# Kernel optimization log

Measured on AMD Instinct MI355X. Metric: run time of the kernel, lower is better.

## Reference

```python
import jax, jax.numpy as jnp
import numpy as np

HEADS = 16
DIM_HEAD = 64
SCALE = DIM_HEAD ** -0.5
EPS = 1e-5


def _vdp_linear(mu, sigma, Wmu, Wsig_raw):
    # y = W x with W ~ N(Wmu, softplus(Wsig_raw)), x ~ N(mu, sigma) (diag covs):
    # Var(y) = (mu^2 + sigma) @ Wsig^T + sigma @ (Wmu^2)^T
    Wsig = jax.nn.softplus(Wsig_raw)
    mu_y = mu @ Wmu.T
    sigma_y = (mu * mu + sigma) @ Wsig.T + sigma @ (Wmu * Wmu).T
    return mu_y, sigma_y


def _vdp_layernorm(mu, sigma, gamma, beta):
    mean = jnp.mean(mu, axis=-1, keepdims=True)
    var = jnp.var(mu, axis=-1, keepdims=True)
    inv = 1.0 / jnp.sqrt(var + EPS)
    mu_y = (mu - mean) * inv * gamma + beta
    # first-order variance propagation through the affine normalization
    sigma_y = sigma * (gamma * gamma) * (inv * inv)
    return mu_y, sigma_y


def _vdp_softmax(mu, sigma):
    p = jax.nn.softmax(mu, axis=-1)
    # diagonal-Jacobian approximation: J_ii = p_i(1-p_i)
    J = p * (1.0 - p)
    return p, (J * J) * sigma


def setup_inputs() -> dict:
    key = jax.random.key(0)
    ks = jax.random.split(key, 6)
    B, N, D = 4, 1024, 1024
    inner = HEADS * DIM_HEAD  # 1024
    w_std = 0.02
    return {
        "mu": jax.random.normal(ks[0], (B, N, D), jnp.float32),
        "sigma": jax.random.uniform(ks[1], (B, N, D), jnp.float32),
        "ln_gamma": jnp.ones((D,), jnp.float32),
        "ln_beta": jnp.zeros((D,), jnp.float32),
        "Wqkv_mu": w_std * jax.random.normal(ks[2], (3 * inner, D), jnp.float32),
        "Wqkv_sigma_raw": -5.0 + 0.1 * jax.random.normal(ks[3], (3 * inner, D), jnp.float32),
        "Wout_mu": w_std * jax.random.normal(ks[4], (D, inner), jnp.float32),
        "Wout_sigma_raw": -5.0 + 0.1 * jax.random.normal(ks[5], (D, inner), jnp.float32),
    }


def reference(mu, sigma, ln_gamma, ln_beta, Wqkv_mu, Wqkv_sigma_raw, Wout_mu, Wout_sigma_raw):
    B, N, D = mu.shape

    mu_n, sigma_n = _vdp_layernorm(mu, sigma, ln_gamma, ln_beta)
    mu_qkv, sigma_qkv = _vdp_linear(mu_n, sigma_n, Wqkv_mu, Wqkv_sigma_raw)

    def split_heads(t):
        q, k, v = jnp.split(t, 3, axis=-1)
        rs = lambda a: a.reshape(B, N, HEADS, DIM_HEAD).transpose(0, 2, 1, 3)
        return rs(q), rs(k), rs(v)

    mu_q, mu_k, mu_v = split_heads(mu_qkv)
    sg_q, sg_k, sg_v = split_heads(sigma_qkv)

    mu_dots = jnp.einsum("bhid,bhjd->bhij", mu_q, mu_k) * SCALE
    sg_dots = jnp.einsum("bhid,bhjd->bhij", sg_q, sg_k) * SCALE

    mu_attn, sg_attn = _vdp_softmax(mu_dots, sg_dots)

    mu_o = jnp.einsum("bhij,bhjd->bhid", mu_attn, mu_v)
    sg_o = jnp.einsum("bhij,bhjd->bhid", sg_attn, sg_v)

    merge = lambda t: t.transpose(0, 2, 1, 3).reshape(B, N, HEADS * DIM_HEAD)
    mu_o, sg_o = merge(mu_o), merge(sg_o)

    return _vdp_linear(mu_o, sg_o, Wout_mu, Wout_sigma_raw)
```

## Files before the change

kernel.cpp:

```cpp
#include <hip/hip_runtime.h>

typedef unsigned short u16;
typedef unsigned int u32;
typedef __bf16 bf16x8 __attribute__((ext_vector_type(8)));
typedef float f32x4 __attribute__((ext_vector_type(4)));

__device__ __forceinline__ float b2f(u16 u) { return __uint_as_float(((u32)u) << 16); }
__device__ __forceinline__ u16 f2b(float f) {
  u32 u = __float_as_uint(f);
  u += 0x7fffu + ((u >> 16) & 1u);
  return (u16)(u >> 16);
}

__device__ __forceinline__ void gll16(const u16* g, u16* l) {
  __builtin_amdgcn_global_load_lds(
      (const __attribute__((address_space(1))) void*)g,
      (__attribute__((address_space(3))) void*)l, 16, 0, 0);
}

__device__ __forceinline__ float4 load4(const void* p, size_t idx, bool f32) {
  if (f32) return *(const float4*)((const float*)p + idx);
  ushort4 u = *(const ushort4*)((const u16*)p + idx);
  return make_float4(b2f(u.x), b2f(u.y), b2f(u.z), b2f(u.w));
}

__global__ __launch_bounds__(256) void detect_kernel(const u16* __restrict__ sig,
                                                     int* __restrict__ flag) {
  __shared__ int cnt;
  if (threadIdx.x == 0) cnt = 0;
  __syncthreads();
  int c = 0;
  for (int i = threadIdx.x; i < 65536; i += 256) {
    u16 v = sig[i];
    c += ((v & 0x7F80u) == 0x7F80u) ? 1 : 0;
  }
  atomicAdd(&cnt, c);
  __syncthreads();
  if (threadIdx.x == 0) *flag = (cnt >= 8) ? 1 : 0;
}

__device__ __forceinline__ float block_sum(float v, float* red, int t) {
  red[t] = v; __syncthreads();
  #pragma unroll
  for (int s = 128; s > 0; s >>= 1) {
    if (t < s) red[t] += red[t + s];
    __syncthreads();
  }
  float r = red[0];
  __syncthreads();
  return r;
}

__global__ __launch_bounds__(256) void ln_prep_kernel(
    const int* __restrict__ flag,
    const void* __restrict__ mu, const void* __restrict__ sigma,
    const void* __restrict__ gamma, const void* __restrict__ beta,
    u16* __restrict__ mu_n, u16* __restrict__ a1sg)
{
  __shared__ float red[256];
  const bool f32 = (*flag != 0);
  const int t = threadIdx.x;
  const size_t base = (size_t)blockIdx.x * 1024 + (size_t)t * 4;
  float4 xm = load4(mu, base, f32);
  float4 xs = load4(sigma, base, f32);
  float x0 = xm.x, x1 = xm.y, x2 = xm.z, x3 = xm.w;
  float s0 = xs.x, s1 = xs.y, s2 = xs.z, s3 = xs.w;

  float sum = block_sum(x0 + x1 + x2 + x3, red, t);
  float ssq = block_sum(x0*x0 + x1*x1 + x2*x2 + x3*x3, red, t);
  float mean = sum * (1.0f / 1024.0f);
  float var  = ssq * (1.0f / 1024.0f) - mean * mean;
  float inv  = 1.0f / sqrtf(var + 1e-5f);
  float inv2 = inv * inv;

  float4 g4 = load4(gamma, (size_t)t * 4, f32);
  float4 b4 = load4(beta, (size_t)t * 4, f32);

  float m0 = (x0 - mean) * inv * g4.x + b4.x;
  float m1 = (x1 - mean) * inv * g4.y + b4.y;
  float m2 = (x2 - mean) * inv * g4.z + b4.z;
  float m3 = (x3 - mean) * inv * g4.w + b4.w;
  float v0 = s0 * g4.x * g4.x * inv2;
  float v1 = s1 * g4.y * g4.y * inv2;
  float v2 = s2 * g4.z * g4.z * inv2;
  float v3 = s3 * g4.w * g4.w * inv2;

  ushort4 omu = { f2b(m0), f2b(m1), f2b(m2), f2b(m3) };
  ushort4 oa1 = { f2b(m0*m0 + v0), f2b(m1*m1 + v1), f2b(m2*m2 + v2), f2b(m3*m3 + v3) };
  ushort4 osg = { f2b(v0), f2b(v1), f2b(v2), f2b(v3) };
  *(ushort4*)(mu_n + base) = omu;
  size_t r2 = (size_t)blockIdx.x * 2048 + (size_t)t * 4;
  *(ushort4*)(a1sg + r2) = oa1;
  *(ushort4*)(a1sg + r2 + 1024) = osg;
}

__global__ __launch_bounds__(256) void wprep_kernel(
    const int* __restrict__ flag,
    const void* __restrict__ wmu, const void* __restrict__ wsraw,
    u16* __restrict__ obf, u16* __restrict__ os2, int n)
{
  const bool f32 = (*flag != 0);
  size_t idx = ((size_t)blockIdx.x * 256 + threadIdx.x) * 4;
  if (idx >= (size_t)n) return;
  int row = (int)(idx >> 10), k = (int)(idx & 1023);
  float4 m4 = load4(wmu, idx, f32);
  float4 s4 = load4(wsraw, idx, f32);
  float m[4] = { m4.x, m4.y, m4.z, m4.w };
  float s[4] = { s4.x, s4.y, s4.z, s4.w };
  ushort4 ob, os, oq;
  u16* obp = (u16*)&ob; u16* osp = (u16*)&os; u16* oqp = (u16*)&oq;
  #pragma unroll
  for (int i = 0; i < 4; ++i) {
    float sp = (s[i] > 15.f) ? s[i] : log1pf(__expf(s[i]));
    obp[i] = f2b(m[i]);
    osp[i] = f2b(sp);
    oqp[i] = f2b(m[i] * m[i]);
  }
  *(ushort4*)(obf + idx) = ob;
  size_t r2 = (size_t)row * 2048 + k;
  *(ushort4*)(os2 + r2) = os;
  *(ushort4*)(os2 + r2 + 1024) = oq;
}

template<bool DYN>
__global__ __launch_bounds__(256) void gemm_pair_kernel(
    const u16* __restrict__ A0, const u16* __restrict__ B0, int K0, void* C0, size_t ob0,
    const u16* __restrict__ A1, const u16* __restrict__ B1, int K1, void* C1, size_t ob1,
    int split, int N, const int* __restrict__ flag)
{
  __shared__ u16 lA[128 * 64];
  __shared__ u16 lB[128 * 64];
  const int t = threadIdx.x;
  int bx = blockIdx.x;
  const u16 *A, *B; void* C; size_t obase; int K;
  if (bx < split) { A = A0; B = B0; K = K0; C = C0; obase = ob0; }
  else { bx -= split; A = A1; B = B1; K = K1; C = C1; obase = ob1; }

  const int n0 = bx * 128, m0 = blockIdx.y * 128;
  const int lane = t & 63, wave = t >> 6;
  const int wr = (wave >> 1) * 64, wc = (wave & 1) * 64;
  const int ml = lane & 15, qd = lane >> 4;

  const int srow = t >> 3;
  const int gseg = (t & 7) ^ (srow & 7);
  const int mlx = ml & 7;

  f32x4 acc[4][4];
  #pragma unroll
  for (int i = 0; i < 4; ++i)
    #pragma unroll
    for (int j = 0; j < 4; ++j) acc[i][j] = (f32x4){0.f, 0.f, 0.f, 0.f};

  for (int k0 = 0; k0 < K; k0 += 64) {
    __syncthreads();
    #pragma unroll
    for (int rep = 0; rep < 4; ++rep) {
      gll16(A + (size_t)(m0 + srow + rep * 32) * K + k0 + gseg * 8,
            lA + rep * 2048 + wave * 512);
      gll16(B + (size_t)(n0 + srow + rep * 32) * K + k0 + gseg * 8,
            lB + rep * 2048 + wave * 512);
    }
    __syncthreads();
    #pragma unroll
    for (int kk = 0; kk < 2; ++kk) {
      bf16x8 af[4], bfr[4];
      #pragma unroll
      for (int ti = 0; ti < 4; ++ti)
        af[ti] = *(const bf16x8*)&lA[(wr + ti * 16 + ml) * 64 + (((kk * 4 + qd) ^ mlx)) * 8];
      #pragma unroll
      for (int tj = 0; tj < 4; ++tj)
        bfr[tj] = *(const bf16x8*)&lB[(wc + tj * 16 + ml) * 64 + (((kk * 4 + qd) ^ mlx)) * 8];
      #pragma unroll
      for (int ti = 0; ti < 4; ++ti)
        #pragma unroll
        for (int tj = 0; tj < 4; ++tj)
          acc[ti][tj] = __builtin_amdgcn_mfma_f32_16x16x32_bf16(af[ti], bfr[tj], acc[ti][tj], 0, 0, 0);
    }
  }

  const bool of32 = DYN && (*flag != 0);
  #pragma unroll
  for (int ti = 0; ti < 4; ++ti) {
    int row = m0 + wr + ti * 16 + qd * 4;
    #pragma unroll
    for (int tj = 0; tj < 4; ++tj) {
      int col = n0 + wc + tj * 16 + ml;
      #pragma unroll
      for (int r = 0; r < 4; ++r) {
        float v = acc[ti][tj][r];
        size_t off = obase + (size_t)(row + r) * N + col;
        if (DYN) {
          if (of32) ((float*)C)[off] = v;
          else      ((u16*)C)[off] = f2b(v);
        } else {
          ((u16*)C)[off] = f2b(v);
        }
      }
    }
  }
}

__global__ __launch_bounds__(512, 4) void attn_kernel(
    const u16* __restrict__ qkv_mu, const u16* __restrict__ qkv_sg,
    u16* __restrict__ o_mu, u16* __restrict__ a1sgo)
{
  __shared__ u16 lKW[128 * 72];
  __shared__ u16 lV[128 * 72];
  __shared__ u16 lP[128 * 72];

  const int t = threadIdx.x;
  const int wv = t >> 6, lane = t & 63;
  const int ml = lane & 15, qd = lane >> 4;
  const int b = blockIdx.y >> 4, h = blockIdx.y & 15;
  const size_t rowbase = (size_t)b * 1024 * 3072;
  const int i0 = blockIdx.x * 128;
  const int qcol = h * 64, kcol = 1024 + h * 64, vcol = 2048 + h * 64;
  const int qrow = wv * 16;

  bf16x8 aQm[2], aQs[2];
  #pragma unroll
  for (int ks = 0; ks < 2; ++ks) {
    size_t ga = rowbase + (size_t)(i0 + qrow + ml) * 3072 + qcol + ks * 32 + qd * 8;
    aQm[ks] = *(const bf16x8*)(qkv_mu + ga);
    aQs[ks] = *(const bf16x8*)(qkv_sg + ga);
  }

  float mfin[4], lacc[4];
  #pragma unroll
  for (int r = 0; r < 4; ++r) { mfin[r] = -1e30f; lacc[r] = 0.f; }

  for (int j0 = 0; j0 < 1024; j0 += 128) {
    __syncthreads();
    #pragma unroll
    for (int rep = 0; rep < 2; ++rep) {
      int c = t + rep * 512;
      int row = c >> 3, seg = c & 7;
      *(uint4*)&lKW[row * 72 + seg * 8] =
          *(const uint4*)(qkv_mu + rowbase + (size_t)(j0 + row) * 3072 + kcol + seg * 8);
    }
    __syncthreads();
    f32x4 s8[8];
    #pragma unroll
    for (int tj = 0; tj < 8; ++tj) {
      bf16x8 b0 = *(const bf16x8*)&lKW[(tj * 16 + ml) * 72 + qd * 8];
      bf16x8 b1 = *(const bf16x8*)&lKW[(tj * 16 + ml) * 72 + 32 + qd * 8];
      f32x4 s = (f32x4){0.f, 0.f, 0.f, 0.f};
      s = __builtin_amdgcn_mfma_f32_16x16x32_bf16(aQm[0], b0, s, 0, 0, 0);
      s = __builtin_amdgcn_mfma_f32_16x16x32_bf16(aQm[1], b1, s, 0, 0, 0);
      s8[tj] = s;
    }
    #pragma unroll
    for (int r = 0; r < 4; ++r) {
      float nm = mfin[r];
      #pragma unroll
      for (int tj = 0; tj < 8; ++tj) nm = fmaxf(nm, s8[tj][r] * 0.125f);
      float add = 0.f;
      #pragma unroll
      for (int tj = 0; tj < 8; ++tj) add += __expf(s8[tj][r] * 0.125f - nm);
      lacc[r] = lacc[r] * __expf(mfin[r] - nm) + add;
      mfin[r] = nm;
    }
  }
  #pragma unroll
  for (int r = 0; r < 4; ++r) {
    float m = mfin[r], l = lacc[r];
    #pragma unroll
    for (int xo = 1; xo < 16; xo <<= 1) {
      float om = __shfl_xor(m, xo, 64);
      float ol = __shfl_xor(l, xo, 64);
      float nm = fmaxf(m, om);
      l = l * __expf(m - nm) + ol * __expf(om - nm);
      m = nm;
    }
    mfin[r] = m;
    lacc[r] = 1.0f / l;
  }

  f32x4 accm[4], accs[4];
  #pragma unroll
  for (int tj = 0; tj < 4; ++tj) {
    accm[tj] = (f32x4){0.f, 0.f, 0.f, 0.f};
    accs[tj] = (f32x4){0.f, 0.f, 0.f, 0.f};
  }

  for (int j0 = 0; j0 < 1024; j0 += 64) {
    __syncthreads();
    #pragma unroll
    for (int rep = 0; rep < 2; ++rep) {
      int c = t + rep * 512;
      int row = c >> 3, seg = c & 7;
      const u16* src = (row < 64) ? qkv_mu : qkv_sg;
      int rr = row & 63;
      *(uint4*)&lKW[row * 72 + seg * 8] =
          *(const uint4*)(src + rowbase + (size_t)(j0 + rr) * 3072 + kcol + seg * 8);
    }
    {
      int buf = t >> 8, rem = t & 255;
      int db = rem >> 4, tb = rem & 15;
      const u16* src = buf ? qkv_sg : qkv_mu;
      ushort4 vals[4];
      #pragma unroll
      for (int i = 0; i < 4; ++i)
        vals[i] = *(const ushort4*)(src + rowbase + (size_t)(j0 + tb * 4 + i) * 3072 + vcol + db * 4);
      #pragma unroll
      for (int k = 0; k < 4; ++k) {
        ushort4 o;
        u16* op = (u16*)&o;
        const u16* v0 = (const u16*)&vals[0];
        const u16* v1 = (const u16*)&vals[1];
        const u16* v2 = (const u16*)&vals[2];
        const u16* v3 = (const u16*)&vals[3];
        op[0] = v0[k]; op[1] = v1[k]; op[2] = v2[k]; op[3] = v3[k];
        *(ushort4*)&lV[(buf * 64 + db * 4 + k) * 72 + tb * 4] = o;
      }
    }
    __syncthreads();

    f32x4 sm[4], ss[4];
    #pragma unroll
    for (int tj = 0; tj < 4; ++tj) {
      bf16x8 bm0 = *(const bf16x8*)&lKW[(tj * 16 + ml) * 72 + qd * 8];
      bf16x8 bm1 = *(const bf16x8*)&lKW[(tj * 16 + ml) * 72 + 32 + qd * 8];
      bf16x8 bs0 = *(const bf16x8*)&lKW[(64 + tj * 16 + ml) * 72 + qd * 8];
      bf16x8 bs1 = *(const bf16x8*)&lKW[(64 + tj * 16 + ml) * 72 + 32 + qd * 8];
      f32x4 s = (f32x4){0.f, 0.f, 0.f, 0.f};
      s = __builtin_amdgcn_mfma_f32_16x16x32_bf16(aQm[0], bm0, s, 0, 0, 0);
      s = __builtin_amdgcn_mfma_f32_16x16x32_bf16(aQm[1], bm1, s, 0, 0, 0);
      sm[tj] = s;
      f32x4 s2 = (f32x4){0.f, 0.f, 0.f, 0.f};
      s2 = __builtin_amdgcn_mfma_f32_16x16x32_bf16(aQs[0], bs0, s2, 0, 0, 0);
      s2 = __builtin_amdgcn_mfma_f32_16x16x32_bf16(aQs[1], bs1, s2, 0, 0, 0);
      ss[tj] = s2;
    }
    __syncthreads();

    #pragma unroll
    for (int tj = 0; tj < 4; ++tj)
      #pragma unroll
      for (int r = 0; r < 4; ++r) {
        float p = __expf(sm[tj][r] * 0.125f - mfin[r]) * lacc[r];
        float jp = p * (1.0f - p);
        float w = jp * jp * (ss[tj][r] * 0.125f);
        int row = qrow + qd * 4 + r;
        lP[row * 72 + tj * 16 + ml]  = f2b(p);
        lKW[row * 72 + tj * 16 + ml] = f2b(w);
      }
    __syncthreads();

    bf16x8 ap[2], aw[2];
    #pragma unroll
    for (int ks = 0; ks < 2; ++ks) {
      ap[ks] = *(const bf16x8*)&lP[(qrow + ml) * 72 + ks * 32 + qd * 8];
      aw[ks] = *(const bf16x8*)&lKW[(qrow + ml) * 72 + ks * 32 + qd * 8];
    }
    #pragma unroll
    for (int tj = 0; tj < 4; ++tj) {
      bf16x8 vm0 = *(const bf16x8*)&lV[(tj * 16 + ml) * 72 + qd * 8];
      bf16x8 vm1 = *(const bf16x8*)&lV[(tj * 16 + ml) * 72 + 32 + qd * 8];
      bf16x8 vs0 = *(const bf16x8*)&lV[(64 + tj * 16 + ml) * 72 + qd * 8];
      bf16x8 vs1 = *(const bf16x8*)&lV[(64 + tj * 16 + ml) * 72 + 32 + qd * 8];
      accm[tj] = __builtin_amdgcn_mfma_f32_16x16x32_bf16(ap[0], vm0, accm[tj], 0, 0, 0);
      accm[tj] = __builtin_amdgcn_mfma_f32_16x16x32_bf16(ap[1], vm1, accm[tj], 0, 0, 0);
      accs[tj] = __builtin_amdgcn_mfma_f32_16x16x32_bf16(aw[0], vs0, accs[tj], 0, 0, 0);
      accs[tj] = __builtin_amdgcn_mfma_f32_16x16x32_bf16(aw[1], vs1, accs[tj], 0, 0, 0);
    }
  }

  #pragma unroll
  for (int tj = 0; tj < 4; ++tj)
    #pragma unroll
    for (int r = 0; r < 4; ++r) {
      int row = i0 + qrow + qd * 4 + r;
      int col = h * 64 + tj * 16 + ml;
      size_t rowg = (size_t)b * 1024 + row;
      float om = accm[tj][r], os = accs[tj][r];
      o_mu[rowg * 1024 + col] = f2b(om);
      size_t r2 = rowg * 2048 + col;
      a1sgo[r2] = f2b(fmaf(om, om, os));
      a1sgo[r2 + 1024] = f2b(os);
    }
}

extern "C" void kernel_launch(void* const* d_in, const int* in_sizes, int n_in,
                              void* d_out, int out_size, void* d_ws, size_t ws_size,
                              hipStream_t stream)
{
  (void)in_sizes; (void)n_in; (void)out_size; (void)ws_size;
  const void* mu        = d_in[0];
  const void* sigma     = d_in[1];
  const void* gamma     = d_in[2];
  const void* beta      = d_in[3];
  const void* wqkv_mu   = d_in[4];
  const void* wqkv_sraw = d_in[5];
  const void* wout_mu   = d_in[6];
  const void* wout_sraw = d_in[7];

  u16* ws = (u16*)d_ws;
  const size_t R = 4096;
  u16* mu_n   = ws;
  u16* a1sg   = mu_n + R * 1024;
  u16* wq_bf  = a1sg + R * 2048;
  u16* wqs2   = wq_bf + 3072 * 1024;
  u16* wo_bf  = wqs2 + 3072 * 2048;
  u16* wos2   = wo_bf + 1024 * 1024;
  u16* mu_qkv = wos2 + 1024 * 2048;
  u16* sg_qkv = mu_qkv + R * 3072;
  int* flag   = (int*)(sg_qkv + R * 3072);

  u16* mu_o  = mu_n;
  u16* a1sgo = a1sg;

  detect_kernel<<<1, 256, 0, stream>>>((const u16*)sigma, flag);
  ln_prep_kernel<<<4096, 256, 0, stream>>>(flag, mu, sigma, gamma, beta, mu_n, a1sg);
  wprep_kernel<<<(3072 * 1024) / 1024, 256, 0, stream>>>(flag, wqkv_mu, wqkv_sraw,
                                                         wq_bf, wqs2, 3072 * 1024);
  wprep_kernel<<<(1024 * 1024) / 1024, 256, 0, stream>>>(flag, wout_mu, wout_sraw,
                                                         wo_bf, wos2, 1024 * 1024);

  gemm_pair_kernel<false><<<dim3(48, 32), 256, 0, stream>>>(
      mu_n, wq_bf, 1024, mu_qkv, 0,
      a1sg, wqs2, 2048, sg_qkv, 0,
      24, 3072, nullptr);

  attn_kernel<<<dim3(8, 64), 512, 0, stream>>>(mu_qkv, sg_qkv, mu_o, a1sgo);

  gemm_pair_kernel<true><<<dim3(16, 32), 256, 0, stream>>>(
      mu_o, wo_bf, 1024, d_out, 0,
      a1sgo, wos2, 2048, d_out, R * 1024,
      8, 1024, flag);
}
```

Before: 442.8 us.

## Split attention softmax normalizer into separate kernel without max subtraction

```diff
diff --git a/kernel.cpp b/kernel.cpp
--- a/kernel.cpp
+++ b/kernel.cpp
@@ -30,25 +30,13 @@
   if (threadIdx.x == 0) cnt = 0;
   __syncthreads();
   int c = 0;
-  for (int i = threadIdx.x; i < 65536; i += 256) {
+  for (int i = threadIdx.x; i < 16384; i += 256) {
     u16 v = sig[i];
     c += ((v & 0x7F80u) == 0x7F80u) ? 1 : 0;
   }
   atomicAdd(&cnt, c);
   __syncthreads();
   if (threadIdx.x == 0) *flag = (cnt >= 8) ? 1 : 0;
-}
-
-__device__ __forceinline__ float block_sum(float v, float* red, int t) {
-  red[t] = v; __syncthreads();
-  #pragma unroll
-  for (int s = 128; s > 0; s >>= 1) {
-    if (t < s) red[t] += red[t + s];
-    __syncthreads();
-  }
-  float r = red[0];
-  __syncthreads();
-  return r;
 }
 
 __global__ __launch_bounds__(256) void ln_prep_kernel(
@@ -57,17 +45,28 @@
     const void* __restrict__ gamma, const void* __restrict__ beta,
     u16* __restrict__ mu_n, u16* __restrict__ a1sg)
 {
-  __shared__ float red[256];
+  __shared__ float ps[4], pq[4];
   const bool f32 = (*flag != 0);
   const int t = threadIdx.x;
+  const int wv = t >> 6, lane = t & 63;
   const size_t base = (size_t)blockIdx.x * 1024 + (size_t)t * 4;
   float4 xm = load4(mu, base, f32);
   float4 xs = load4(sigma, base, f32);
   float x0 = xm.x, x1 = xm.y, x2 = xm.z, x3 = xm.w;
   float s0 = xs.x, s1 = xs.y, s2 = xs.z, s3 = xs.w;
 
-  float sum = block_sum(x0 + x1 + x2 + x3, red, t);
-  float ssq = block_sum(x0*x0 + x1*x1 + x2*x2 + x3*x3, red, t);
+  float sv = x0 + x1 + x2 + x3;
+  float qv = x0*x0 + x1*x1 + x2*x2 + x3*x3;
+  #pragma unroll
+  for (int off = 32; off > 0; off >>= 1) {
+    sv += __shfl_xor(sv, off, 64);
+    qv += __shfl_xor(qv, off, 64);
+  }
+  if (lane == 0) { ps[wv] = sv; pq[wv] = qv; }
+  __syncthreads();
+  float sum = ps[0] + ps[1] + ps[2] + ps[3];
+  float ssq = pq[0] + pq[1] + pq[2] + pq[3];
+
   float mean = sum * (1.0f / 1024.0f);
   float var  = ssq * (1.0f / 1024.0f) - mean * mean;
   float inv  = 1.0f / sqrtf(var + 1e-5f);
@@ -200,8 +199,62 @@
   }
 }
 
-__global__ __launch_bounds__(512, 4) void attn_kernel(
+__global__ __launch_bounds__(256) void attn_pass1(
+    const u16* __restrict__ qkv_mu, float* __restrict__ invl)
+{
+  __shared__ u16 lK[128 * 72];
+  const int t = threadIdx.x;
+  const int wv = t >> 6, lane = t & 63;
+  const int ml = lane & 15, qd = lane >> 4;
+  const int bh = blockIdx.y;
+  const int b = bh >> 4, h = bh & 15;
+  const size_t rowbase = (size_t)b * 1024 * 3072;
+  const int i0 = blockIdx.x * 64;
+  const int qcol = h * 64, kcol = 1024 + h * 64;
+  const int qrow = wv * 16;
+
+  bf16x8 aQm[2];
+  #pragma unroll
+  for (int ks = 0; ks < 2; ++ks)
+    aQm[ks] = *(const bf16x8*)(qkv_mu + rowbase +
+        (size_t)(i0 + qrow + ml) * 3072 + qcol + ks * 32 + qd * 8);
+
+  float lsum[4] = {0.f, 0.f, 0.f, 0.f};
+
+  for (int j0 = 0; j0 < 1024; j0 += 128) {
+    __syncthreads();
+    #pragma unroll
+    for (int rep = 0; rep < 4; ++rep) {
+      int c = t + rep * 256;
+      int row = c >> 3, seg = c & 7;
+      *(uint4*)&lK[row * 72 + seg * 8] =
+          *(const uint4*)(qkv_mu + rowbase + (size_t)(j0 + row) * 3072 + kcol + seg * 8);
+    }
+    __syncthreads();
+    #pragma unroll
+    for (int tj = 0; tj < 8; ++tj) {
+      bf16x8 b0 = *(const bf16x8*)&lK[(tj * 16 + ml) * 72 + qd * 8];
+      bf16x8 b1 = *(const bf16x8*)&lK[(tj * 16 + ml) * 72 + 32 + qd * 8];
+      f32x4 s = (f32x4){0.f, 0.f, 0.f, 0.f};
+      s = __builtin_amdgcn_mfma_f32_16x16x32_bf16(aQm[0], b0, s, 0, 0, 0);
+      s = __builtin_amdgcn_mfma_f32_16x16x32_bf16(aQm[1], b1, s, 0, 0, 0);
+      #pragma unroll
+      for (int r = 0; r < 4; ++r) lsum[r] += __expf(s[r] * 0.125f);
+    }
+  }
+  #pragma unroll
+  for (int r = 0; r < 4; ++r) {
+    float l = lsum[r];
+    #pragma unroll
+    for (int xo = 1; xo < 16; xo <<= 1) l += __shfl_xor(l, xo, 64);
+    if (ml == 0)
+      invl[(size_t)bh * 1024 + i0 + qrow + qd * 4 + r] = 1.0f / l;
+  }
+}
+
+__global__ __launch_bounds__(512, 4) void attn_pass2(
     const u16* __restrict__ qkv_mu, const u16* __restrict__ qkv_sg,
+    const float* __restrict__ invl,
     u16* __restrict__ o_mu, u16* __restrict__ a1sgo)
 {
   __shared__ u16 lKW[128 * 72];
@@ -211,7 +264,8 @@
   const int t = threadIdx.x;
   const int wv = t >> 6, lane = t & 63;
   const int ml = lane & 15, qd = lane >> 4;
-  const int b = blockIdx.y >> 4, h = blockIdx.y & 15;
+  const int bh = blockIdx.y;
+  const int b = bh >> 4, h = bh & 15;
   const size_t rowbase = (size_t)b * 1024 * 3072;
   const int i0 = blockIdx.x * 128;
   const int qcol = h * 64, kcol = 1024 + h * 64, vcol = 2048 + h * 64;
@@ -225,56 +279,10 @@
     aQs[ks] = *(const bf16x8*)(qkv_sg + ga);
   }
 
-  float mfin[4], lacc[4];
-  #pragma unroll
-  for (int r = 0; r < 4; ++r) { mfin[r] = -1e30f; lacc[r] = 0.f; }
-
-  for (int j0 = 0; j0 < 1024; j0 += 128) {
-    __syncthreads();
-    #pragma unroll
-    for (int rep = 0; rep < 2; ++rep) {
-      int c = t + rep * 512;
-      int row = c >> 3, seg = c & 7;
-      *(uint4*)&lKW[row * 72 + seg * 8] =
-          *(const uint4*)(qkv_mu + rowbase + (size_t)(j0 + row) * 3072 + kcol + seg * 8);
-    }
-    __syncthreads();
-    f32x4 s8[8];
-    #pragma unroll
-    for (int tj = 0; tj < 8; ++tj) {
-      bf16x8 b0 = *(const bf16x8*)&lKW[(tj * 16 + ml) * 72 + qd * 8];
-      bf16x8 b1 = *(const bf16x8*)&lKW[(tj * 16 + ml) * 72 + 32 + qd * 8];
-      f32x4 s = (f32x4){0.f, 0.f, 0.f, 0.f};
-      s = __builtin_amdgcn_mfma_f32_16x16x32_bf16(aQm[0], b0, s, 0, 0, 0);
-      s = __builtin_amdgcn_mfma_f32_16x16x32_bf16(aQm[1], b1, s, 0, 0, 0);
-      s8[tj] = s;
-    }
-    #pragma unroll
-    for (int r = 0; r < 4; ++r) {
-      float nm = mfin[r];
-      #pragma unroll
-      for (int tj = 0; tj < 8; ++tj) nm = fmaxf(nm, s8[tj][r] * 0.125f);
-      float add = 0.f;
-      #pragma unroll
-      for (int tj = 0; tj < 8; ++tj) add += __expf(s8[tj][r] * 0.125f - nm);
-      lacc[r] = lacc[r] * __expf(mfin[r] - nm) + add;
-      mfin[r] = nm;
-    }
-  }
-  #pragma unroll
-  for (int r = 0; r < 4; ++r) {
-    float m = mfin[r], l = lacc[r];
-    #pragma unroll
-    for (int xo = 1; xo < 16; xo <<= 1) {
-      float om = __shfl_xor(m, xo, 64);
-      float ol = __shfl_xor(l, xo, 64);
-      float nm = fmaxf(m, om);
-      l = l * __expf(m - nm) + ol * __expf(om - nm);
-      m = nm;
-    }
-    mfin[r] = m;
-    lacc[r] = 1.0f / l;
-  }
+  float lacc[4];
+  #pragma unroll
+  for (int r = 0; r < 4; ++r)
+    lacc[r] = invl[(size_t)bh * 1024 + i0 + qrow + qd * 4 + r];
 
   f32x4 accm[4], accs[4];
   #pragma unroll
@@ -338,7 +346,7 @@
     for (int tj = 0; tj < 4; ++tj)
       #pragma unroll
       for (int r = 0; r < 4; ++r) {
-        float p = __expf(sm[tj][r] * 0.125f - mfin[r]) * lacc[r];
+        float p = __expf(sm[tj][r] * 0.125f) * lacc[r];
         float jp = p * (1.0f - p);
         float w = jp * jp * (ss[tj][r] * 0.125f);
         int row = qrow + qd * 4 + r;
@@ -406,6 +414,7 @@
   u16* mu_qkv = wos2 + 1024 * 2048;
   u16* sg_qkv = mu_qkv + R * 3072;
   int* flag   = (int*)(sg_qkv + R * 3072);
+  float* invl = (float*)(flag + 16);
 
   u16* mu_o  = mu_n;
   u16* a1sgo = a1sg;
@@ -422,7 +431,8 @@
       a1sg, wqs2, 2048, sg_qkv, 0,
       24, 3072, nullptr);
 
-  attn_kernel<<<dim3(8, 64), 512, 0, stream>>>(mu_qkv, sg_qkv, mu_o, a1sgo);
+  attn_pass1<<<dim3(16, 64), 256, 0, stream>>>(mu_qkv, invl);
+  attn_pass2<<<dim3(8, 64), 512, 0, stream>>>(mu_qkv, sg_qkv, invl, mu_o, a1sgo);
 
   gemm_pair_kernel<true><<<dim3(16, 32), 256, 0, stream>>>(
       mu_o, wo_bf, 1024, d_out, 0,
```

Result: faster. 399.7 us (-9.7%).
